# Kernel tuning notes

Hardware: AMD Instinct MI355X
Metric: run time of the kernel (lower is better)

## Reference

```python
import jax, jax.numpy as jnp
import numpy as np

V, E, H, B, S, C = 50000, 300, 512, 128, 80, 6
HH = 2 * H  # hidden_dim * num_directions (BiDi=True)


def _gru_dir(x, w_ih, w_hh, b_ih, b_hh, reverse):
    # x: (b, t, e) -> (b, t, h); torch nn.GRU cell math
    Bv, T, _ = x.shape
    Hd = w_hh.shape[1]
    xg = jnp.einsum('bte,ge->btg', x, w_ih) + b_ih  # (b, t, 3h)
    if reverse:
        xg = xg[:, ::-1]
    def step(h, xt):
        gi_r, gi_z, gi_n = jnp.split(xt, 3, axis=-1)
        gh_r, gh_z, gh_n = jnp.split(h @ w_hh.T + b_hh, 3, axis=-1)
        r = jax.nn.sigmoid(gi_r + gh_r)
        z = jax.nn.sigmoid(gi_z + gh_z)
        n = jnp.tanh(gi_n + r * gh_n)
        hn = (1.0 - z) * n + z * h
        return hn, hn
    h0 = jnp.zeros((Bv, Hd), x.dtype)
    _, hs = jax.lax.scan(step, h0, jnp.swapaxes(xg, 0, 1))
    hs = jnp.swapaxes(hs, 0, 1)
    if reverse:
        hs = hs[:, ::-1]
    return hs


def _bigru(x, pf, pb):
    return jnp.concatenate([_gru_dir(x, *pf, reverse=False), _gru_dir(x, *pb, reverse=True)], axis=-1)


def _conv1d(x, w, b, d):
    y = jax.lax.conv_general_dilated(x, w, (1,), 'VALID', rhs_dilation=(d,),
                                     dimension_numbers=('NCH', 'OIH', 'NCH'))
    return y + b[None, :, None]


def _bn(x, g, b, m, v):
    # eval-mode BatchNorm1d with running stats
    return (x - m[None, :, None]) * (g[None, :, None] / jnp.sqrt(v[None, :, None] + 1e-5)) + b[None, :, None]


def setup_inputs():
    key = jax.random.key(0)
    ks = iter(jax.random.split(key, 64))
    def W(*shape):
        return jax.random.normal(next(ks), shape, jnp.float32) * 0.02
    inp = {
        'input_batch': jax.random.randint(next(ks), (B, S), 1, V),
        'choices_batch': jax.random.randint(next(ks), (B, 4, C), 1, V),
        'emb_table': W(V, E),
    }
    for p in ('sg', 'cg'):
        for d in ('f', 'b'):
            inp[p + '_wih_' + d] = W(3 * H, E)
            inp[p + '_whh_' + d] = W(3 * H, H)
            inp[p + '_bih_' + d] = W(3 * H)
            inp[p + '_bhh_' + d] = W(3 * H)
    inp['lin_w'] = W(HH, HH * C)
    inp['lin_b'] = W(HH)
    inp['attn_w'] = W(HH, HH)
    inp['attn_b'] = W(HH)
    inp['c11_w'] = W(HH, S, 3);  inp['c11_b'] = W(HH)
    inp['c13_w'] = W(HH, HH, 3); inp['c13_b'] = W(HH)
    inp['c21_w'] = W(HH, HH, 3); inp['c21_b'] = W(HH)
    inp['c23_w'] = W(HH, HH, 3); inp['c23_b'] = W(HH)
    for i in ('1', '2'):
        inp['bn' + i + '_g'] = jnp.ones((HH,), jnp.float32)
        inp['bn' + i + '_b'] = jnp.zeros((HH,), jnp.float32)
        inp['bn' + i + '_m'] = jnp.zeros((HH,), jnp.float32)
        inp['bn' + i + '_v'] = jnp.ones((HH,), jnp.float32)
    inp['gate_wp'] = W(2 * HH, HH)
    inp['gate_wc'] = W(2 * HH, 2 * HH)
    inp['gate_b'] = W(2 * HH)
    inp['out_wp'] = W(2 * HH, HH)
    inp['out_b'] = W(2 * HH)
    return inp


def reference(input_batch, choices_batch, emb_table,
              sg_wih_f, sg_whh_f, sg_bih_f, sg_bhh_f, sg_wih_b, sg_whh_b, sg_bih_b, sg_bhh_b,
              cg_wih_f, cg_whh_f, cg_bih_f, cg_bhh_f, cg_wih_b, cg_whh_b, cg_bih_b, cg_bhh_b,
              lin_w, lin_b, attn_w, attn_b,
              c11_w, c11_b, c13_w, c13_b, c21_w, c21_b, c23_w, c23_b,
              bn1_g, bn1_b, bn1_m, bn1_v, bn2_g, bn2_b, bn2_m, bn2_v,
              gate_wp, gate_wc, gate_b, out_wp, out_b):
    # --- encode passage: embedding + BiGRU (dropout is eval-mode identity) ---
    sent = _bigru(emb_table[input_batch],
                  (sg_wih_f, sg_whh_f, sg_bih_f, sg_bhh_f),
                  (sg_wih_b, sg_whh_b, sg_bih_b, sg_bhh_b))  # (B, S, 2h)
    cgf = (cg_wih_f, cg_whh_f, cg_bih_f, cg_bhh_f)
    cgb = (cg_wih_b, cg_whh_b, cg_bih_b, cg_bhh_b)

    def choice_vec(tok):  # (B, C) -> (B, 2h)
        g = _bigru(emb_table[tok], cgf, cgb)               # (B, C, 2h)
        return g.reshape(g.shape[0], -1) @ lin_w.T + lin_b

    cvs = [choice_vec(choices_batch[:, i]) for i in range(4)]

    # --- AttnReader: shared Wh/bh, per-choice softmax attention over seq ---
    Wh = jnp.einsum('bsh,hg->bsg', sent, attn_w)  # (B, S, 2h)
    bh = sent @ attn_b                            # (B, S)

    def attn_read(cv):
        a = jax.nn.softmax(jnp.einsum('bsg,bg->bs', Wh, cv) + bh, axis=1)
        return jnp.einsum('bs,bsh->bh', a, sent)  # (B, 2h)

    pars = [attn_read(cv) for cv in cvs]

    # --- IDCNN: Conv1d treats seq dim S as channels (faithful to source) ---
    x = jax.nn.relu(_bn(_conv1d(sent, c11_w, c11_b, 1), bn1_g, bn1_b, bn1_m, bn1_v))
    x = _conv1d(x, c13_w, c13_b, 3)
    x = jax.nn.relu(_bn(_conv1d(x, c21_w, c21_b, 1), bn2_g, bn2_b, bn2_m, bn2_v))
    x = _conv1d(x, c23_w, c23_b, 3)
    P = jnp.max(x, axis=2)  # AdaptiveMaxPool1d(1) + squeeze -> (B, 2h)

    Cs = [jnp.concatenate([cv, par], axis=1) for cv, par in zip(cvs, pars)]  # (B, 4h)

    # --- PointerNet (note: source bug makes out1..out4 all equal C1WP+bC1) ---
    WP = P @ gate_wp.T          # (B, 4h)
    WP_out = P @ out_wp.T       # (B, 4h)
    Cd1 = Cs[0] * jax.nn.sigmoid(WP + Cs[0] @ gate_wc.T + gate_b)
    o1 = jnp.sum(Cd1 * WP_out, axis=1, keepdims=True) + (Cd1 @ out_b)[:, None]  # (B, 1)
    return jnp.concatenate([o1, o1, o1, o1], axis=1)  # (B, 4)
```

## Files before the change

kernel.cpp:

```cpp
#include <hip/hip_runtime.h>

typedef unsigned int u32;
typedef unsigned short u16;
typedef __attribute__((ext_vector_type(4))) float f32x4;
typedef __attribute__((ext_vector_type(8))) short bf16x8;

#define DEV static __device__ __forceinline__

DEV float sigf(float x){ return 1.0f/(1.0f + expf(-x)); }

DEV u16 f2bf(float x){
  u32 u = __float_as_uint(x);
  u32 r = (u + 0x7FFFu + ((u >> 16) & 1u)) >> 16;
  return (u16)r;
}

DEV u32 encf(float f){
  u32 u = __float_as_uint(f);
  return (u & 0x80000000u) ? ~u : (u | 0x80000000u);
}
DEV float decf(u32 e){
  return (e & 0x80000000u) ? __uint_as_float(e ^ 0x80000000u) : __uint_as_float(~e);
}

DEV void gload16(const void* g, void* l){
  __builtin_amdgcn_global_load_lds((const __attribute__((address_space(1))) u32*)g,
                                   (__attribute__((address_space(3))) u32*)l, 16, 0, 0);
}

__global__ __launch_bounds__(256,2) void gemm_bf16(
    const u16* __restrict__ A, const u16* __restrict__ A2,
    const u16* __restrict__ B,
    const float* __restrict__ bias, const float* __restrict__ bias2,
    float* __restrict__ C, float* __restrict__ C2, int ldc,
    int Kp, int ksteps)
{
  __shared__ u16 lds[(128 + 128)*32];
  char* ldsc = (char*)&lds[0];
  const int Boff = 128*64;
  const int tid = threadIdx.x;
  const int l = tid & 63, w = tid >> 6;
  const int n0 = blockIdx.x * 128, m0 = blockIdx.y * 128;
  const u16* Ause = blockIdx.z ? A2 : A;
  const float* buse = blockIdx.z ? bias2 : bias;
  float* Cuse = blockIdx.z ? C2 : C;
  const int wr = w >> 1, wc = w & 1;
  const int lr = l & 15, g = l >> 4;

  f32x4 acc[4][4];
  #pragma unroll
  for (int i=0;i<4;++i)
    #pragma unroll
    for (int j=0;j<4;++j) acc[i][j] = f32x4{0.f,0.f,0.f,0.f};

  for (int ks = 0; ks < ksteps; ++ks) {
    const int i0 = ks*32;
    __syncthreads();
    #pragma unroll
    for (int r = 0; r < 2; ++r) {
      const int rr = w*2 + r;
      const int c = rr*64 + l;
      const int row = c >> 2, bpos = c & 3;
      const int ib = bpos ^ ((row>>1) & 3);
      gload16(Ause + ((size_t)(m0 + row)*Kp + (i0 + ib*8)), ldsc + rr*1024);
      gload16(B    + ((size_t)(n0 + row)*Kp + (i0 + ib*8)), ldsc + Boff + rr*1024);
    }
    __syncthreads();
    bf16x8 af[4], bfr[4];
    #pragma unroll
    for (int m=0;m<4;++m){
      int o = wr*64 + m*16 + lr;
      af[m] = *(const bf16x8*)(ldsc + o*64 + ((g ^ ((o>>1)&3))<<4));
    }
    #pragma unroll
    for (int n=0;n<4;++n){
      int pr = wc*64 + n*16 + lr;
      bfr[n] = *(const bf16x8*)(ldsc + Boff + pr*64 + ((g ^ ((pr>>1)&3))<<4));
    }
    #pragma unroll
    for (int m=0;m<4;++m)
      #pragma unroll
      for (int n=0;n<4;++n)
        acc[m][n] = __builtin_amdgcn_mfma_f32_16x16x32_bf16(af[m], bfr[n], acc[m][n], 0,0,0);
  }

  #pragma unroll
  for (int m=0;m<4;++m){
    int mm = m0 + wr*64 + m*16 + g*4;
    f32x4 bv = *(const f32x4*)(buse + mm);
    #pragma unroll
    for (int n=0;n<4;++n){
      int p = n0 + wc*64 + n*16 + lr;
      f32x4 v;
      #pragma unroll
      for (int r2=0;r2<4;++r2) v[r2] = acc[m][n][r2] + bv[r2];
      *(f32x4*)(Cuse + (size_t)p*ldc + mm) = v;
    }
  }
}

__global__ __launch_bounds__(256,2) void gemm_bf16_sk(
    const u16* __restrict__ A, const u16* __restrict__ B,
    float* __restrict__ C, int ldc, int Kp, int kpc)
{
  __shared__ u16 lds[(128 + 128)*32];
  char* ldsc = (char*)&lds[0];
  const int Boff = 128*64;
  const int tid = threadIdx.x;
  const int l = tid & 63, w = tid >> 6;
  const int n0 = blockIdx.x * 128, m0 = blockIdx.y * 128;
  const int ks0 = blockIdx.z * kpc;
  const int wr = w >> 1, wc = w & 1;
  const int lr = l & 15, g = l >> 4;

  f32x4 acc[4][4];
  #pragma unroll
  for (int i=0;i<4;++i)
    #pragma unroll
    for (int j=0;j<4;++j) acc[i][j] = f32x4{0.f,0.f,0.f,0.f};

  for (int ks = 0; ks < kpc; ++ks) {
    const int i0 = (ks0 + ks)*32;
    __syncthreads();
    #pragma unroll
    for (int r = 0; r < 2; ++r) {
      const int rr = w*2 + r;
      const int c = rr*64 + l;
      const int row = c >> 2, bpos = c & 3;
      const int ib = bpos ^ ((row>>1) & 3);
      gload16(A + ((size_t)(m0 + row)*Kp + (i0 + ib*8)), ldsc + rr*1024);
      gload16(B + ((size_t)(n0 + row)*Kp + (i0 + ib*8)), ldsc + Boff + rr*1024);
    }
    __syncthreads();
    bf16x8 af[4], bfr[4];
    #pragma unroll
    for (int m=0;m<4;++m){
      int o = wr*64 + m*16 + lr;
      af[m] = *(const bf16x8*)(ldsc + o*64 + ((g ^ ((o>>1)&3))<<4));
    }
    #pragma unroll
    for (int n=0;n<4;++n){
      int pr = wc*64 + n*16 + lr;
      bfr[n] = *(const bf16x8*)(ldsc + Boff + pr*64 + ((g ^ ((pr>>1)&3))<<4));
    }
    #pragma unroll
    for (int m=0;m<4;++m)
      #pragma unroll
      for (int n=0;n<4;++n)
        acc[m][n] = __builtin_amdgcn_mfma_f32_16x16x32_bf16(af[m], bfr[n], acc[m][n], 0,0,0);
  }

  #pragma unroll
  for (int m=0;m<4;++m){
    int mm = m0 + wr*64 + m*16 + g*4;
    #pragma unroll
    for (int n=0;n<4;++n){
      int p = n0 + wc*64 + n*16 + lr;
      float* dst = C + (size_t)p*ldc + mm;
      #pragma unroll
      for (int r2=0;r2<4;++r2) atomicAdd(dst + r2, acc[m][n][r2]);
    }
  }
}

__global__ void initc(float* __restrict__ C, const float* __restrict__ bias,
                      int total, int mmask)
{
  int i = blockIdx.x*256 + threadIdx.x;
  if (i < total) C[i] = bias ? bias[i & mmask] : 0.f;
}

__global__ __launch_bounds__(256) void gru_step(
    const float* __restrict__ xg0, const float* __restrict__ xg1,
    const float* __restrict__ whh0, const float* __restrict__ whh1,
    const float* __restrict__ bhh0, const float* __restrict__ bhh1,
    float* __restrict__ hs, int S, int t)
{
  __shared__ float hL[32*520];
  __shared__ float wL[48*132];
  const int tid = threadIdx.x;
  const int tj = tid & 15, tb = tid >> 4;
  const int jg = blockIdx.x;
  const int b0 = blockIdx.y*32;
  const int dir = blockIdx.z;
  const int l = tid & 63, w = tid >> 6;
  const float* xg  = dir ? xg1  : xg0;
  const float* whh = dir ? whh1 : whh0;
  const float* bhh = dir ? bhh1 : bhh0;
  const int tt = dir ? (S-1-t) : t;
  const int j = jg*16 + tj;

  float accr[2], accz[2], accn[2];
  {
    float br = bhh[j], bz = bhh[512+j], bn = bhh[1024+j];
    accr[0]=br; accr[1]=br; accz[0]=bz; accz[1]=bz; accn[0]=bn; accn[1]=bn;
  }

  if (t > 0){
    const int tp = dir ? (tt+1) : (tt-1);
    #pragma unroll
    for (int rr = 0; rr < 8; ++rr){
      int row = w*8 + rr;
      const float* srcb = hs + ((size_t)(b0+row)*S + tp)*1024 + dir*512;
      gload16(srcb + l*4,       (char*)hL + (size_t)(row*520)*4);
      gload16(srcb + 256 + l*4, (char*)hL + (size_t)(row*520 + 256)*4);
    }
    for (int c = 0; c < 4; ++c){
      const int k0 = c*128;
      __syncthreads();
      #pragma unroll
      for (int i = 0; i < 6; ++i){
        int qidx = tid + i*256;
        int row = qidx >> 5, q = qidx & 31;
        int grow = (row>>4)*512 + jg*16 + (row & 15);
        f32x4 v = *(const f32x4*)(whh + (size_t)grow*512 + k0 + q*4);
        *(f32x4*)(wL + row*132 + q*4) = v;
      }
      __syncthreads();
      #pragma unroll 4
      for (int q = 0; q < 32; ++q){
        f32x4 ha  = *(const f32x4*)(hL + (2*tb  )*520 + k0 + q*4);
        f32x4 hb  = *(const f32x4*)(hL + (2*tb+1)*520 + k0 + q*4);
        f32x4 wr4 = *(const f32x4*)(wL + tj*132      + q*4);
        f32x4 wz4 = *(const f32x4*)(wL + (16+tj)*132 + q*4);
        f32x4 wn4 = *(const f32x4*)(wL + (32+tj)*132 + q*4);
        #pragma unroll
        for (int e = 0; e < 4; ++e){
          accr[0] += ha[e]*wr4[e]; accz[0] += ha[e]*wz4[e]; accn[0] += ha[e]*wn4[e];
          accr[1] += hb[e]*wr4[e]; accz[1] += hb[e]*wz4[e]; accn[1] += hb[e]*wn4[e];
        }
      }
    }
  }

  #pragma unroll
  for (int bi = 0; bi < 2; ++bi){
    int lb = 2*tb + bi;
    int b = b0 + lb;
    size_t xbase = ((size_t)b*S + tt)*1536;
    float gir = xg[xbase + j], giz = xg[xbase + 512 + j], gin = xg[xbase + 1024 + j];
    float hp = (t>0) ? hL[lb*520 + j] : 0.f;
    float r = sigf(gir + accr[bi]);
    float z = sigf(giz + accz[bi]);
    float n = tanhf(gin + r*accn[bi]);
    hs[((size_t)b*S + tt)*1024 + dir*512 + j] = (1.f - z)*n + z*hp;
  }
}

__global__ void transpose_sent(const float* __restrict__ sent, u16* __restrict__ sentT)
{
  __shared__ float tl[80][65];
  int b = blockIdx.y, h0 = blockIdx.x*64;
  for (int idx = threadIdx.x; idx < 80*64; idx += 256){
    int s = idx >> 6, hh = idx & 63;
    tl[s][hh] = sent[((size_t)b*80 + s)*1024 + h0 + hh];
  }
  __syncthreads();
  for (int idx = threadIdx.x; idx < 64*96; idx += 256){
    int hh = idx / 96, s = idx % 96;
    sentT[((size_t)b*1024 + h0 + hh)*96 + s] = (s < 80) ? f2bf(tl[s][hh]) : (u16)0;
  }
}

__global__ void attn_scores(const float* __restrict__ sent, const float* __restrict__ u,
                            const float* __restrict__ attn_b, float* __restrict__ sc)
{
  int wid = blockIdx.x*4 + (threadIdx.x >> 6);
  int lane = threadIdx.x & 63;
  const float* row = sent + (size_t)wid*1024;
  const float* ub = u + (size_t)(wid/80)*1024;
  float acc = 0.f;
  for (int h = lane; h < 1024; h += 64) acc += row[h]*(ub[h] + attn_b[h]);
  #pragma unroll
  for (int m = 32; m; m >>= 1) acc += __shfl_xor(acc, m);
  if (lane == 0) sc[wid] = acc;
}

__global__ void softmax80(const float* __restrict__ sc, float* __restrict__ a)
{
  int b = blockIdx.x, l = threadIdx.x;
  float v0 = sc[b*80 + l];
  float v1 = (l < 16) ? sc[b*80 + 64 + l] : -1e30f;
  float mx = fmaxf(v0, v1);
  #pragma unroll
  for (int m = 32; m; m >>= 1) mx = fmaxf(mx, __shfl_xor(mx, m));
  float e0 = expf(v0 - mx);
  float e1 = (l < 16) ? expf(v1 - mx) : 0.f;
  float s = e0 + e1;
  #pragma unroll
  for (int m = 32; m; m >>= 1) s += __shfl_xor(s, m);
  float inv = 1.f/s;
  a[b*80 + l] = e0*inv;
  if (l < 16) a[b*80 + 64 + l] = e1*inv;
}

__global__ void par_cs0(const float* __restrict__ a, const float* __restrict__ sent,
                        const float* __restrict__ cv, float* __restrict__ Cs0)
{
  int b = blockIdx.x;
  for (int h = threadIdx.x; h < 1024; h += 256){
    float acc = 0.f;
    for (int s = 0; s < 80; ++s) acc += a[b*80+s]*sent[((size_t)b*80+s)*1024 + h];
    Cs0[(size_t)b*2048 + 1024 + h] = acc;
    Cs0[(size_t)b*2048 + h] = cv[(size_t)b*1024 + h];
  }
}

__global__ void pack_w(const float* __restrict__ src, u16* __restrict__ dst,
                       int O, int CIs, int CIp)
{
  int i = blockIdx.x*256 + threadIdx.x;
  int total = 3*O*CIp;
  if (i >= total) return;
  int tap = i/(O*CIp); int rem = i%(O*CIp); int o = rem/CIp, ci = rem%CIp;
  float v = (ci < CIs) ? src[((size_t)o*CIs + ci)*3 + tap] : 0.f;
  dst[((size_t)tap*O + o)*CIp + ci] = f2bf(v);
}

__global__ void pack_wk(const float* __restrict__ src, u16* __restrict__ dst,
                        int M, int Ks, int Kp)
{
  int i = blockIdx.x*256 + threadIdx.x;
  if (i >= M*Kp) return;
  int row = i/Kp, k = i%Kp;
  dst[i] = (k < Ks) ? f2bf(src[(size_t)row*Ks + k]) : (u16)0;
}

__global__ void pack_f2b(const float* __restrict__ src, u16* __restrict__ dst, int n)
{
  int i = blockIdx.x*256 + threadIdx.x;
  if (i < n) dst[i] = f2bf(src[i]);
}

__global__ void pack_x(const float* __restrict__ emb, const int* __restrict__ toks,
                       int rdiv, int rmul, u16* __restrict__ dst, int R)
{
  int i = blockIdx.x*256 + threadIdx.x;
  if (i >= R*320) return;
  int row = i/320, k = i%320;
  int tok = toks[(row/rdiv)*rmul + (row%rdiv)];
  dst[i] = (k < 300) ? f2bf(emb[(size_t)tok*300 + k]) : (u16)0;
}

__global__ void prep_ab(const float* c11b, const float* c13b, const float* c21b, const float* c23b,
                        const float* g1, const float* b1, const float* m1, const float* v1,
                        const float* g2, const float* b2, const float* m2, const float* v2,
                        float* ab)
{
  int i = blockIdx.x*256 + threadIdx.x;
  if (i >= 4096) return;
  int layer = i >> 10, o = i & 1023;
  float al, be;
  if (layer == 0){ al = g1[o]/sqrtf(v1[o]+1e-5f); be = c11b[o]*al + b1[o] - m1[o]*al; }
  else if (layer == 1){ al = 1.f; be = c13b[o]; }
  else if (layer == 2){ al = g2[o]/sqrtf(v2[o]+1e-5f); be = c21b[o]*al + b2[o] - m2[o]*al; }
  else { al = 1.f; be = c23b[o]; }
  ab[layer*2048 + o] = al;
  ab[layer*2048 + 1024 + o] = be;
}

__global__ void init_penc(u32* p){
  int i = blockIdx.x*256 + threadIdx.x;
  if (i < 128*1024) p[i] = encf(-3.3e38f);
}
__global__ void dec_p(const u32* __restrict__ pe, float* __restrict__ pf){
  int i = blockIdx.x*256 + threadIdx.x;
  if (i < 128*1024) pf[i] = decf(pe[i]);
}

#define CONV_STAGE(DST, I0)                                                   \
  {                                                                           \
    _Pragma("unroll")                                                         \
    for (int r = 0; r < 6; ++r) {                                             \
      const int c = r*512 + tid;                                              \
      const int row = c >> 2, bpos = c & 3;                                   \
      const int tap = row >> 8, o = row & 255;                                \
      const int ib = bpos ^ ((row>>1) & 3);                                   \
      gload16(Wt + ((size_t)(tap*1024 + o0 + o)*CI + ((I0) + ib*8)),          \
              (DST) + (size_t)c*16);                                          \
    }                                                                         \
    _Pragma("unroll")                                                         \
    for (int r = 0; r < 2; ++r) {                                             \
      const int c = w*136 + r*64 + l;                                         \
      const int row = c >> 2, bpos = c & 3;                                   \
      const int ib = bpos ^ ((row>>1) & 3);                                   \
      int ps = p0 + row; ps = ps < P_in ? ps : (P_in - 1);                    \
      gload16(Xb + ((size_t)ps*CI + ((I0) + ib*8)),                           \
              (DST) + BOFF + (size_t)c*16);                                   \
    }                                                                         \
    if (l < 8) {                                                              \
      const int c = w*136 + 128 + l;                                          \
      const int row = c >> 2, bpos = c & 3;                                   \
      const int ib = bpos ^ ((row>>1) & 3);                                   \
      int ps = p0 + row; ps = ps < P_in ? ps : (P_in - 1);                    \
      gload16(Xb + ((size_t)ps*CI + ((I0) + ib*8)),                           \
              (DST) + BOFF + (size_t)c*16);                                   \
    }                                                                         \
  }

__global__ __launch_bounds__(512,2) void conv_mfma(
    const u16* __restrict__ X, long bstrideX,
    const u16* __restrict__ Wt,
    const float* __restrict__ alpha, const float* __restrict__ beta,
    u16* __restrict__ Y, long bstrideY,
    u32* __restrict__ Penc, int b0,
    int P_in, int P_out, int CI, int dil, int ksteps, int mode)
{
  __shared__ u16 lds[66560];
  char* ldsc = (char*)&lds[0];
  const int BUF = 66560;
  const int BOFF = 768*64;
  const int tid = threadIdx.x;
  const int l = tid & 63, w = tid >> 6;
  const int wg = blockIdx.x + (blockIdx.y<<2) + (blockIdx.z<<4);
  const int id2 = ((wg & 7) << 5) | (wg >> 3);
  const int p0 = (id2 & 3) * 256;
  const int o0 = ((id2 >> 2) & 3) * 256;
  const int bz = id2 >> 4;
  const u16* Xb = X + (size_t)bz * (size_t)bstrideX;
  const int wr = w >> 2, wc = w & 3;
  const int lr = l & 15, g = l >> 4;

  f32x4 acc[8][4];
  #pragma unroll
  for (int i=0;i<8;++i)
    #pragma unroll
    for (int j=0;j<4;++j) acc[i][j] = f32x4{0.f,0.f,0.f,0.f};

  CONV_STAGE(ldsc, 0)

  for (int ks = 0; ks < ksteps; ++ks) {
    const int cur = ks & 1;
    if (ks + 1 < ksteps) {
      char* dst = ldsc + (cur^1)*BUF;
      CONV_STAGE(dst, (ks+1)*32)
      asm volatile("s_waitcnt vmcnt(9)" ::: "memory");
    } else {
      asm volatile("s_waitcnt vmcnt(0)" ::: "memory");
    }
    __builtin_amdgcn_s_barrier();
    asm volatile("" ::: "memory");

    char* src = ldsc + cur*BUF;
    __builtin_amdgcn_s_setprio(1);
    #pragma unroll
    for (int tap = 0; tap < 3; ++tap) {
      bf16x8 af[8];
      #pragma unroll
      for (int m=0;m<8;++m){
        int o = wr*128 + m*16 + lr;
        int row = tap*256 + o;
        af[m] = *(const bf16x8*)(src + row*64 + ((g ^ ((row>>1)&3))<<4));
      }
      #pragma unroll
      for (int n=0;n<4;++n){
        int pr = wc*64 + n*16 + lr + dil*tap;
        bf16x8 bfr = *(const bf16x8*)(src + BOFF + pr*64 + ((g ^ ((pr>>1)&3))<<4));
        #pragma unroll
        for (int m=0;m<8;++m)
          acc[m][n] = __builtin_amdgcn_mfma_f32_16x16x32_bf16(af[m], bfr, acc[m][n], 0,0,0);
      }
    }
    __builtin_amdgcn_s_setprio(0);

    asm volatile("s_waitcnt lgkmcnt(0)" ::: "memory");
    __builtin_amdgcn_s_barrier();
    asm volatile("" ::: "memory");
  }

  if (mode == 2) {
    #pragma unroll
    for (int m=0;m<8;++m){
      int oo = o0 + wr*128 + m*16 + g*4;
      f32x4 al = *(const f32x4*)(alpha + oo);
      f32x4 be = *(const f32x4*)(beta + oo);
      float vm[4] = {-1e30f,-1e30f,-1e30f,-1e30f};
      #pragma unroll
      for (int n=0;n<4;++n){
        int p = p0 + wc*64 + n*16 + lr;
        bool ok = p < P_out;
        #pragma unroll
        for (int r2=0;r2<4;++r2){
          float v = acc[m][n][r2]*al[r2] + be[r2];
          vm[r2] = ok ? fmaxf(vm[r2], v) : vm[r2];
        }
      }
      #pragma unroll
      for (int r2=0;r2<4;++r2){
        float v = vm[r2];
        #pragma unroll
        for (int mask=1; mask<16; mask<<=1) v = fmaxf(v, __shfl_xor(v, mask));
        if (lr == 0) atomicMax(&Penc[(size_t)(b0+bz)*1024 + oo + r2], encf(v));
      }
    }
  } else {
    #pragma unroll
    for (int m=0;m<8;++m){
      int oo = o0 + wr*128 + m*16 + g*4;
      f32x4 al = *(const f32x4*)(alpha + oo);
      f32x4 be = *(const f32x4*)(beta + oo);
      #pragma unroll
      for (int n=0;n<4;++n){
        int p = p0 + wc*64 + n*16 + lr;
        if (p < P_out){
          float v0 = acc[m][n][0]*al[0] + be[0];
          float v1 = acc[m][n][1]*al[1] + be[1];
          float v2 = acc[m][n][2]*al[2] + be[2];
          float v3 = acc[m][n][3]*al[3] + be[3];
          if (mode == 0){ v0=fmaxf(v0,0.f); v1=fmaxf(v1,0.f); v2=fmaxf(v2,0.f); v3=fmaxf(v3,0.f); }
          uint2 pk;
          pk.x = (u32)f2bf(v0) | ((u32)f2bf(v1) << 16);
          pk.y = (u32)f2bf(v2) | ((u32)f2bf(v3) << 16);
          *(uint2*)(Y + (size_t)bz*(size_t)bstrideY + (size_t)p*1024 + oo) = pk;
        }
      }
    }
  }
}

__global__ void head_final(const float* __restrict__ Cs0, const float* __restrict__ t1,
                           const float* __restrict__ t2, const float* __restrict__ outb,
                           float* __restrict__ dout)
{
  __shared__ float red[256];
  int b = blockIdx.x;
  float part = 0.f;
  for (int gg = threadIdx.x; gg < 2048; gg += 256){
    float cd = Cs0[(size_t)b*2048+gg] * sigf(t1[(size_t)b*2048+gg]);
    part += cd * (t2[(size_t)b*2048+gg] + outb[gg]);
  }
  red[threadIdx.x] = part;
  __syncthreads();
  for (int s = 128; s > 0; s >>= 1){
    if (threadIdx.x < s) red[threadIdx.x] += red[threadIdx.x + s];
    __syncthreads();
  }
  if (threadIdx.x < 4) dout[b*4 + threadIdx.x] = red[0];
}

extern "C" void kernel_launch(void* const* d_in, const int* in_sizes, int n_in,
                              void* d_out, int out_size, void* d_ws, size_t ws_size,
                              hipStream_t stream)
{
  (void)in_sizes; (void)n_in; (void)out_size; (void)ws_size;
  const int*   input_batch = (const int*)d_in[0];
  const int*   choices     = (const int*)d_in[1];
  const float* emb    = (const float*)d_in[2];
  const float* sgwihf = (const float*)d_in[3];
  const float* sgwhhf = (const float*)d_in[4];
  const float* sgbihf = (const float*)d_in[5];
  const float* sgbhhf = (const float*)d_in[6];
  const float* sgwihb = (const float*)d_in[7];
  const float* sgwhhb = (const float*)d_in[8];
  const float* sgbihb = (const float*)d_in[9];
  const float* sgbhhb = (const float*)d_in[10];
  const float* cgwihf = (const float*)d_in[11];
  const float* cgwhhf = (const float*)d_in[12];
  const float* cgbihf = (const float*)d_in[13];
  const float* cgbhhf = (const float*)d_in[14];
  const float* cgwihb = (const float*)d_in[15];
  const float* cgwhhb = (const float*)d_in[16];
  const float* cgbihb = (const float*)d_in[17];
  const float* cgbhhb = (const float*)d_in[18];
  const float* lin_w  = (const float*)d_in[19];
  const float* lin_b  = (const float*)d_in[20];
  const float* attn_w = (const float*)d_in[21];
  const float* attn_b = (const float*)d_in[22];
  const float* c11w = (const float*)d_in[23];
  const float* c11b = (const float*)d_in[24];
  const float* c13w = (const float*)d_in[25];
  const float* c13b = (const float*)d_in[26];
  const float* c21w = (const float*)d_in[27];
  const float* c21b = (const float*)d_in[28];
  const float* c23w = (const float*)d_in[29];
  const float* c23b = (const float*)d_in[30];
  const float* bn1g = (const float*)d_in[31];
  const float* bn1b = (const float*)d_in[32];
  const float* bn1m = (const float*)d_in[33];
  const float* bn1v = (const float*)d_in[34];
  const float* bn2g = (const float*)d_in[35];
  const float* bn2b = (const float*)d_in[36];
  const float* bn2m = (const float*)d_in[37];
  const float* bn2v = (const float*)d_in[38];
  const float* gatewp = (const float*)d_in[39];
  const float* gatewc = (const float*)d_in[40];
  const float* gateb  = (const float*)d_in[41];
  const float* outwp  = (const float*)d_in[42];
  const float* outb   = (const float*)d_in[43];
  float* dout = (float*)d_out;

  char* ws = (char*)d_ws; size_t off = 0;
  auto alc = [&](size_t n)->char*{ char* p = ws + off; off = (off + n + 255) & ~(size_t)255; return p; };
  float* xg_f  = (float*)alc((size_t)128*80*1536*4);
  float* xg_b  = (float*)alc((size_t)128*80*1536*4);
  float* xg_cf = (float*)alc((size_t)128*6*1536*4);
  float* xg_cb = (float*)alc((size_t)128*6*1536*4);
  float* gh    = (float*)alc((size_t)2*128*1536*4); (void)gh;
  float* sent  = (float*)alc((size_t)128*80*1024*4);
  float* g_c   = (float*)alc((size_t)128*6*1024*4);
  u16*   sentT = (u16*)alc((size_t)128*1024*96*2);
  float* cv    = (float*)alc((size_t)128*1024*4);
  float* uu    = (float*)alc((size_t)128*1024*4);
  float* scb   = (float*)alc((size_t)128*80*4);
  float* aw    = (float*)alc((size_t)128*80*4);
  float* Cs0   = (float*)alc((size_t)128*2048*4);
  u16* W1p = (u16*)alc((size_t)3*1024*96*2);
  u16* W2p = (u16*)alc((size_t)3*1024*1024*2);
  u16* W3p = (u16*)alc((size_t)3*1024*1024*2);
  u16* W4p = (u16*)alc((size_t)3*1024*1024*2);
  float* ab  = (float*)alc((size_t)4*2048*4);
  u32*  Penc = (u32*)alc((size_t)128*1024*4);
  float* Pf  = (float*)alc((size_t)128*1024*4);
  float* t1  = (float*)alc((size_t)128*2048*4);
  float* t2  = (float*)alc((size_t)128*2048*4);
  u16* xbf_s = (u16*)alc((size_t)10240*320*2);
  u16* xbf_c = (u16*)alc((size_t)768*320*2);
  u16* Wsf = (u16*)alc((size_t)1536*320*2);
  u16* Wsb = (u16*)alc((size_t)1536*320*2);
  u16* Wcf = (u16*)alc((size_t)1536*320*2);
  u16* Wcb = (u16*)alc((size_t)1536*320*2);

  char* R1 = (char*)xg_f;
  u16* linw_bf  = (u16*)(R1);
  u16* attnw_bf = (u16*)(R1 + 12582912);
  u16* gcbf     = (u16*)(R1 + 14680064);
  u16* cvbf     = (u16*)(R1 + 16252928);
  const int bc = 16;
  u16* Y0 = (u16*)(R1 + 16515072);
  u16* Y1 = Y0 + (size_t)bc*1024*1024;
  char* R2 = (char*)sent;
  u16* gwp_bf = (u16*)(R2);
  u16* gwc_bf = (u16*)(R2 + 4194304);
  u16* owp_bf = (u16*)(R2 + 12582912);
  u16* Pfbf   = (u16*)(R2 + 16777216);
  u16* Cs0bf  = (u16*)(R2 + 17039360);

  dim3 T(256), T5(512);

  pack_w<<<dim3((3*1024*96+255)/256), T, 0, stream>>>(c11w, W1p, 1024, 80, 96);
  pack_w<<<dim3((3*1024*1024+255)/256), T, 0, stream>>>(c13w, W2p, 1024, 1024, 1024);
  pack_w<<<dim3((3*1024*1024+255)/256), T, 0, stream>>>(c21w, W3p, 1024, 1024, 1024);
  pack_w<<<dim3((3*1024*1024+255)/256), T, 0, stream>>>(c23w, W4p, 1024, 1024, 1024);
  pack_wk<<<dim3((1536*320+255)/256), T, 0, stream>>>(sgwihf, Wsf, 1536, 300, 320);
  pack_wk<<<dim3((1536*320+255)/256), T, 0, stream>>>(sgwihb, Wsb, 1536, 300, 320);
  pack_wk<<<dim3((1536*320+255)/256), T, 0, stream>>>(cgwihf, Wcf, 1536, 300, 320);
  pack_wk<<<dim3((1536*320+255)/256), T, 0, stream>>>(cgwihb, Wcb, 1536, 300, 320);
  pack_x<<<dim3((10240*320+255)/256), T, 0, stream>>>(emb, input_batch, 80, 80, xbf_s, 10240);
  pack_x<<<dim3((768*320+255)/256), T, 0, stream>>>(emb, choices, 6, 24, xbf_c, 768);
  prep_ab<<<16, T, 0, stream>>>(c11b, c13b, c21b, c23b,
                                bn1g,bn1b,bn1m,bn1v, bn2g,bn2b,bn2m,bn2v, ab);
  init_penc<<<512, T, 0, stream>>>(Penc);

  gemm_bf16<<<dim3(80,12,2), T, 0, stream>>>(Wsf, Wsb, xbf_s, sgbihf, sgbihb,
                                             xg_f, xg_b, 1536, 320, 10);
  gemm_bf16<<<dim3(6,12,2), T, 0, stream>>>(Wcf, Wcb, xbf_c, cgbihf, cgbihb,
                                            xg_cf, xg_cb, 1536, 320, 10);

  for (int t = 0; t < 80; ++t)
    gru_step<<<dim3(32,4,2), T, 0, stream>>>(xg_f, xg_b, sgwhhf, sgwhhb,
                                             sgbhhf, sgbhhb, sent, 80, t);
  for (int t = 0; t < 6; ++t)
    gru_step<<<dim3(32,4,2), T, 0, stream>>>(xg_cf, xg_cb, cgwhhf, cgwhhb,
                                             cgbhhf, cgbhhb, g_c, 6, t);

  pack_wk<<<dim3((1024*6144+255)/256), T, 0, stream>>>(lin_w, linw_bf, 1024, 6144, 6144);
  pack_wk<<<dim3((1024*1024+255)/256), T, 0, stream>>>(attn_w, attnw_bf, 1024, 1024, 1024);
  pack_f2b<<<dim3((128*6144+255)/256), T, 0, stream>>>(g_c, gcbf, 128*6144);

  transpose_sent<<<dim3(16,128), T, 0, stream>>>(sent, sentT);

  initc<<<dim3((128*1024+255)/256), T, 0, stream>>>(cv, lin_b, 128*1024, 1023);
  gemm_bf16_sk<<<dim3(1,8,6), T, 0, stream>>>(linw_bf, gcbf, cv, 1024, 6144, 32);
  pack_f2b<<<dim3((128*1024+255)/256), T, 0, stream>>>(cv, cvbf, 128*1024);
  initc<<<dim3((128*1024+255)/256), T, 0, stream>>>(uu, nullptr, 128*1024, 1023);
  gemm_bf16_sk<<<dim3(1,8,2), T, 0, stream>>>(attnw_bf, cvbf, uu, 1024, 1024, 16);
  attn_scores<<<2560, T, 0, stream>>>(sent, uu, attn_b, scb);
  softmax80<<<128, dim3(64), 0, stream>>>(scb, aw);
  par_cs0<<<128, T, 0, stream>>>(aw, sent, cv, Cs0);

  pack_wk<<<dim3((2048*1024+255)/256), T, 0, stream>>>(gatewp, gwp_bf, 2048, 1024, 1024);
  pack_wk<<<dim3((2048*2048+255)/256), T, 0, stream>>>(gatewc, gwc_bf, 2048, 2048, 2048);
  pack_wk<<<dim3((2048*1024+255)/256), T, 0, stream>>>(outwp, owp_bf, 2048, 1024, 1024);
  pack_f2b<<<dim3((128*2048+255)/256), T, 0, stream>>>(Cs0, Cs0bf, 128*2048);

  for (int b0 = 0; b0 < 128; b0 += bc){
    conv_mfma<<<dim3(4,4,bc), T5, 0, stream>>>(sentT + (size_t)b0*1024*96, (long)1024*96,
        W1p, ab+0,    ab+1024, Y0, (long)1024*1024, nullptr, 0, 1024, 1022, 96,   1, 3,  0);
    conv_mfma<<<dim3(4,4,bc), T5, 0, stream>>>(Y0, (long)1024*1024,
        W2p, ab+2048, ab+3072, Y1, (long)1024*1024, nullptr, 0, 1022, 1016, 1024, 3, 32, 1);
    conv_mfma<<<dim3(4,4,bc), T5, 0, stream>>>(Y1, (long)1024*1024,
        W3p, ab+4096, ab+5120, Y0, (long)1024*1024, nullptr, 0, 1016, 1014, 1024, 1, 32, 0);
    conv_mfma<<<dim3(4,4,bc), T5, 0, stream>>>(Y0, (long)1024*1024,
        W4p, ab+6144, ab+7168, nullptr, 0, Penc, b0,          1014, 1008, 1024, 3, 32, 2);
  }
  dec_p<<<512, T, 0, stream>>>(Penc, Pf);
  pack_f2b<<<dim3((128*1024+255)/256), T, 0, stream>>>(Pf, Pfbf, 128*1024);

  initc<<<dim3((128*2048+255)/256), T, 0, stream>>>(t1, gateb, 128*2048, 2047);
  gemm_bf16_sk<<<dim3(1,16,2), T, 0, stream>>>(gwp_bf, Pfbf, t1, 2048, 1024, 16);
  gemm_bf16_sk<<<dim3(1,16,4), T, 0, stream>>>(gwc_bf, Cs0bf, t1, 2048, 2048, 16);
  initc<<<dim3((128*2048+255)/256), T, 0, stream>>>(t2, nullptr, 128*2048, 2047);
  gemm_bf16_sk<<<dim3(1,16,2), T, 0, stream>>>(owp_bf, Pfbf, t2, 2048, 1024, 16);
  head_final<<<128, T, 0, stream>>>(Cs0, t1, t2, outb, dout);
}
```

Measured before the change: 3.981 ms.

## Pipeline conv MFMA per tap with 4-slot weight ring buffer

Restructures the conv_mfma main loop from a double-buffered K-step (all three taps staged at once) into per-tap phases. Weight tiles go into a 4-slot ring and input tiles are double-buffered, so global loads for the next tap are issued while the current tap's MFMAs run. Load addresses are precomputed once and advanced by pointer increments. LDS usage drops, and there are more barriers per K-step with finer-grained vmcnt waits, which risks correctness in the ring indexing and extra sync overhead.

Result: faster. 3.745 ms (-5.9%).

```diff
diff --git a/kernel.cpp b/kernel.cpp
--- a/kernel.cpp
+++ b/kernel.cpp
@@ -368,35 +368,44 @@
   if (i < 128*1024) pf[i] = decf(pe[i]);
 }
 
-#define CONV_STAGE(DST, I0)                                                   \
+#define CONV_PHASE(TAP, BRD, STAGECODE, WAITCODE)                             \
   {                                                                           \
+    const char* Ab = ldsc + (((ks3 + (TAP)) & 3) << 14) + aRd;                \
+    const char* Bb = ldsc + 65536 + bpar + (BRD);                             \
+    bf16x8 af[8], bfr[4];                                                     \
     _Pragma("unroll")                                                         \
-    for (int r = 0; r < 6; ++r) {                                             \
-      const int c = r*512 + tid;                                              \
-      const int row = c >> 2, bpos = c & 3;                                   \
-      const int tap = row >> 8, o = row & 255;                                \
-      const int ib = bpos ^ ((row>>1) & 3);                                   \
-      gload16(Wt + ((size_t)(tap*1024 + o0 + o)*CI + ((I0) + ib*8)),          \
-              (DST) + (size_t)c*16);                                          \
-    }                                                                         \
+    for (int m=0;m<8;++m) af[m] = *(const bf16x8*)(Ab + m*1024);              \
     _Pragma("unroll")                                                         \
-    for (int r = 0; r < 2; ++r) {                                             \
-      const int c = w*136 + r*64 + l;                                         \
-      const int row = c >> 2, bpos = c & 3;                                   \
-      const int ib = bpos ^ ((row>>1) & 3);                                   \
-      int ps = p0 + row; ps = ps < P_in ? ps : (P_in - 1);                    \
-      gload16(Xb + ((size_t)ps*CI + ((I0) + ib*8)),                           \
-              (DST) + BOFF + (size_t)c*16);                                   \
-    }                                                                         \
-    if (l < 8) {                                                              \
-      const int c = w*136 + 128 + l;                                          \
-      const int row = c >> 2, bpos = c & 3;                                   \
-      const int ib = bpos ^ ((row>>1) & 3);                                   \
-      int ps = p0 + row; ps = ps < P_in ? ps : (P_in - 1);                    \
-      gload16(Xb + ((size_t)ps*CI + ((I0) + ib*8)),                           \
-              (DST) + BOFF + (size_t)c*16);                                   \
-    }                                                                         \
-  }
+    for (int n=0;n<4;++n) bfr[n] = *(const bf16x8*)(Bb + n*1024);             \
+    STAGECODE                                                                 \
+    WAITCODE                                                                  \
+    __builtin_amdgcn_s_setprio(1);                                            \
+    _Pragma("unroll")                                                         \
+    for (int n=0;n<4;++n)                                                     \
+      _Pragma("unroll")                                                       \
+      for (int m=0;m<8;++m)                                                   \
+        acc[m][n] = __builtin_amdgcn_mfma_f32_16x16x32_bf16(af[m], bfr[n],    \
+                                                            acc[m][n],0,0,0); \
+    __builtin_amdgcn_s_setprio(0);                                            \
+    asm volatile("" ::: "memory");                                            \
+    __builtin_amdgcn_s_barrier();                                             \
+    asm volatile("" ::: "memory");                                            \
+  }
+
+#define STAGE_A(TAP)                                                          \
+      {                                                                       \
+        char* Adst = ldsc + (((ks3 + (TAP) + 3) & 3) << 14);                  \
+        gload16(aptr0 + (size_t)(TAP)*1024*CI, Adst + aLd0);                  \
+        gload16(aptr1 + (size_t)(TAP)*1024*CI, Adst + aLd1);                  \
+      }
+
+#define STAGE_B                                                               \
+      {                                                                       \
+        char* Bdst = ldsc + 65536 + (bpar ^ 17408);                           \
+        gload16(bptr0, Bdst + bLd0);                                          \
+        gload16(bptr1, Bdst + bLd1);                                          \
+        if (l < 8) gload16(bptr2, Bdst + bLd2);                               \
+      }
 
 __global__ __launch_bounds__(512,2) void conv_mfma(
     const u16* __restrict__ X, long bstrideX,
@@ -406,10 +415,8 @@
     u32* __restrict__ Penc, int b0,
     int P_in, int P_out, int CI, int dil, int ksteps, int mode)
 {
-  __shared__ u16 lds[66560];
+  __shared__ u16 lds[50176];
   char* ldsc = (char*)&lds[0];
-  const int BUF = 66560;
-  const int BOFF = 768*64;
   const int tid = threadIdx.x;
   const int l = tid & 63, w = tid >> 6;
   const int wg = blockIdx.x + (blockIdx.y<<2) + (blockIdx.z<<4);
@@ -421,51 +428,76 @@
   const int wr = w >> 2, wc = w & 3;
   const int lr = l & 15, g = l >> 4;
 
+  const int aRd  = (wr*128 + lr)*64 + ((g ^ ((lr>>1)&3))<<4);
+  const int bRd0 = (wc*64 + lr)*64 + ((g ^ ((lr>>1)&3))<<4);
+  const int bRd1 = (wc*64 + lr + dil)*64 + ((g ^ (((lr+dil)>>1)&3))<<4);
+  const int bRd2 = (wc*64 + lr + 2*dil)*64 + ((g ^ (((lr+2*dil)>>1)&3))<<4);
+
+  const u16 *aptr0, *aptr1;
+  int aLd0, aLd1;
+  {
+    int c0 = tid,        r0 = c0 >> 2, i0b = (c0 & 3) ^ ((r0>>1)&3);
+    int c1 = 512 + tid,  r1 = c1 >> 2, i1b = (c1 & 3) ^ ((r1>>1)&3);
+    aptr0 = Wt + ((size_t)(o0 + r0)*CI + i0b*8);  aLd0 = c0*16;
+    aptr1 = Wt + ((size_t)(o0 + r1)*CI + i1b*8);  aLd1 = c1*16;
+  }
+  const u16 *bptr0, *bptr1, *bptr2;
+  int bLd0, bLd1, bLd2;
+  {
+    int c0 = w*136 + l,          r0 = c0 >> 2, i0b = (c0 & 3) ^ ((r0>>1)&3);
+    int c1 = w*136 + 64 + l,     r1 = c1 >> 2, i1b = (c1 & 3) ^ ((r1>>1)&3);
+    int c2 = w*136 + 128 + (l&7),r2 = c2 >> 2, i2b = (c2 & 3) ^ ((r2>>1)&3);
+    int p0c = p0 + r0; p0c = p0c < P_in ? p0c : (P_in-1);
+    int p1c = p0 + r1; p1c = p1c < P_in ? p1c : (P_in-1);
+    int p2c = p0 + r2; p2c = p2c < P_in ? p2c : (P_in-1);
+    bptr0 = Xb + ((size_t)p0c*CI + i0b*8);  bLd0 = c0*16;
+    bptr1 = Xb + ((size_t)p1c*CI + i1b*8);  bLd1 = c1*16;
+    bptr2 = Xb + ((size_t)p2c*CI + i2b*8);  bLd2 = c2*16;
+  }
+
   f32x4 acc[8][4];
   #pragma unroll
   for (int i=0;i<8;++i)
     #pragma unroll
     for (int j=0;j<4;++j) acc[i][j] = f32x4{0.f,0.f,0.f,0.f};
 
-  CONV_STAGE(ldsc, 0)
-
-  for (int ks = 0; ks < ksteps; ++ks) {
-    const int cur = ks & 1;
-    if (ks + 1 < ksteps) {
-      char* dst = ldsc + (cur^1)*BUF;
-      CONV_STAGE(dst, (ks+1)*32)
-      asm volatile("s_waitcnt vmcnt(9)" ::: "memory");
-    } else {
-      asm volatile("s_waitcnt vmcnt(0)" ::: "memory");
-    }
-    __builtin_amdgcn_s_barrier();
-    asm volatile("" ::: "memory");
-
-    char* src = ldsc + cur*BUF;
-    __builtin_amdgcn_s_setprio(1);
-    #pragma unroll
-    for (int tap = 0; tap < 3; ++tap) {
-      bf16x8 af[8];
-      #pragma unroll
-      for (int m=0;m<8;++m){
-        int o = wr*128 + m*16 + lr;
-        int row = tap*256 + o;
-        af[m] = *(const bf16x8*)(src + row*64 + ((g ^ ((row>>1)&3))<<4));
-      }
-      #pragma unroll
-      for (int n=0;n<4;++n){
-        int pr = wc*64 + n*16 + lr + dil*tap;
-        bf16x8 bfr = *(const bf16x8*)(src + BOFF + pr*64 + ((g ^ ((pr>>1)&3))<<4));
-        #pragma unroll
-        for (int m=0;m<8;++m)
-          acc[m][n] = __builtin_amdgcn_mfma_f32_16x16x32_bf16(af[m], bfr, acc[m][n], 0,0,0);
-      }
-    }
-    __builtin_amdgcn_s_setprio(0);
-
-    asm volatile("s_waitcnt lgkmcnt(0)" ::: "memory");
-    __builtin_amdgcn_s_barrier();
-    asm volatile("" ::: "memory");
+  {
+    gload16(aptr0, ldsc + aLd0);
+    gload16(aptr1, ldsc + aLd1);
+    gload16(aptr0 + (size_t)1024*CI, ldsc + (1<<14) + aLd0);
+    gload16(aptr1 + (size_t)1024*CI, ldsc + (1<<14) + aLd1);
+    gload16(aptr0 + (size_t)2048*CI, ldsc + (2<<14) + aLd0);
+    gload16(aptr1 + (size_t)2048*CI, ldsc + (2<<14) + aLd1);
+    gload16(bptr0, ldsc + 65536 + bLd0);
+    gload16(bptr1, ldsc + 65536 + bLd1);
+    if (l < 8) gload16(bptr2, ldsc + 65536 + bLd2);
+    aptr0 += 32; aptr1 += 32; bptr0 += 32; bptr1 += 32; bptr2 += 32;
+  }
+  asm volatile("s_waitcnt vmcnt(0)" ::: "memory");
+  __builtin_amdgcn_s_barrier();
+  asm volatile("" ::: "memory");
+
+  int ks3 = 0;
+  for (int ks = 0; ks < ksteps-1; ++ks) {
+    const int bpar = (ks & 1) ? 17408 : 0;
+    CONV_PHASE(0, bRd0,
+      STAGE_A(0) STAGE_B,
+      asm volatile("s_waitcnt vmcnt(7)" ::: "memory");)
+    CONV_PHASE(1, bRd1,
+      STAGE_A(1),
+      asm volatile("s_waitcnt vmcnt(7)" ::: "memory");)
+    CONV_PHASE(2, bRd2,
+      STAGE_A(2)
+      { aptr0 += 32; aptr1 += 32; bptr0 += 32; bptr1 += 32; bptr2 += 32; },
+      asm volatile("s_waitcnt vmcnt(4)" ::: "memory");)
+    ks3 += 3;
+  }
+  {
+    const int bpar = ((ksteps-1) & 1) ? 17408 : 0;
+    CONV_PHASE(0, bRd0, {},
+      asm volatile("s_waitcnt vmcnt(0)" ::: "memory");)
+    CONV_PHASE(1, bRd1, {}, {})
+    CONV_PHASE(2, bRd2, {}, {})
   }
 
   if (mode == 2) {
```
